# Kernel tuning notes

Measured on AMD Instinct MI355X. Metric: run time of the kernel, lower is better.

The kernel has to match this reference:

```python
import jax, jax.numpy as jnp
import numpy as np

B, S, H, V = 32, 512, 768, 30522
N_UPDATE, MAX_LEN = 3, 8
NEG_INF = -1e9


def setup_inputs() -> dict:
    key = jax.random.key(0)
    ks = jax.random.split(key, 12)
    x = jax.random.randint(ks[0], (B, S), 0, V, dtype=jnp.int32)
    decoder_input = jax.random.normal(ks[1], (B, N_UPDATE, H), dtype=jnp.float32)
    encoder_output = jax.random.normal(ks[2], (B, S, H), dtype=jnp.float32)
    hidden = jax.random.normal(ks[3], (1, B, H), dtype=jnp.float32)
    teacher = jax.random.randint(ks[4], (B, N_UPDATE, MAX_LEN), 0, V, dtype=jnp.int32)
    # tied embedding table, padding_idx=0 row zeroed
    embed_w = (jax.random.normal(ks[5], (V, H), dtype=jnp.float32) * 0.02).at[0].set(0.0)
    # GRU weights ~ N(0, initializer_range=0.02), biases zero (torch default biases exist; keep small random)
    gru_w_ih = jax.random.normal(ks[6], (3 * H, H), dtype=jnp.float32) * 0.02
    gru_w_hh = jax.random.normal(ks[7], (3 * H, H), dtype=jnp.float32) * 0.02
    gru_b_ih = jax.random.normal(ks[8], (3 * H,), dtype=jnp.float32) * 0.02
    gru_b_hh = jax.random.normal(ks[9], (3 * H,), dtype=jnp.float32) * 0.02
    wgen_w = jax.random.normal(ks[10], (1, 3 * H), dtype=jnp.float32) * 0.02
    wgen_b = jnp.zeros((1,), dtype=jnp.float32)
    return {"x": x, "decoder_input": decoder_input, "encoder_output": encoder_output,
            "hidden": hidden, "teacher": teacher, "embed_w": embed_w,
            "gru_w_ih": gru_w_ih, "gru_w_hh": gru_w_hh, "gru_b_ih": gru_b_ih,
            "gru_b_hh": gru_b_hh, "wgen_w": wgen_w, "wgen_b": wgen_b, "max_len": MAX_LEN}


def _gru_cell(w, h, w_ih, w_hh, b_ih, b_hh):
    # PyTorch GRU cell. w, h: [B, H]
    gi = w @ w_ih.T + b_ih  # [B, 3H]
    gh = h @ w_hh.T + b_hh
    i_r, i_z, i_n = jnp.split(gi, 3, axis=-1)
    h_r, h_z, h_n = jnp.split(gh, 3, axis=-1)
    r = jax.nn.sigmoid(i_r + h_r)
    z = jax.nn.sigmoid(i_z + h_z)
    n = jnp.tanh(i_n + r * h_n)
    return (1.0 - z) * n + z * h


def reference(x, decoder_input, encoder_output, hidden, teacher, embed_w,
              gru_w_ih, gru_w_hh, gru_b_ih, gru_b_hh, wgen_w, wgen_b, max_len):
    b, n_update, hid = decoder_input.shape
    vocab = embed_w.shape[0]
    mask = (x == 0)  # [B, S]
    bidx = jnp.arange(b)[:, None]

    # Teacher-forced inputs: step 0 of slot j uses decoder_input[:, j];
    # step k>0 uses embed(teacher[:, j, k-1]).
    teacher_emb = embed_w[teacher]                     # [B, nU, L, H]
    inputs = jnp.concatenate([decoder_input[:, :, None, :], teacher_emb[:, :, :-1, :]], axis=2)
    inputs = inputs.transpose(1, 2, 0, 3).reshape(n_update * max_len, b, hid)  # [nU*L, B, H]

    h0 = hidden[0]  # [B, H]

    def step(h, w):
        h = _gru_cell(w, h, gru_w_ih, gru_w_hh, gru_b_ih, gru_b_hh)
        attn_e = jnp.einsum('bsh,bh->bs', encoder_output, h)
        attn_e = jnp.where(mask, NEG_INF, attn_e)
        attn_history = jax.nn.softmax(attn_e, axis=-1)          # [B, S]
        attn_vocab = jax.nn.softmax(h @ embed_w.T, axis=-1)     # [B, V]
        context = jnp.einsum('bs,bsh->bh', attn_history, encoder_output)
        p_gen = jax.nn.sigmoid(jnp.concatenate([w, h, context], axis=-1) @ wgen_w.T + wgen_b)  # [B,1]
        p_ctx = jnp.zeros((b, vocab), dtype=attn_vocab.dtype).at[bidx, x].add(attn_history)
        p_final = p_gen * attn_vocab + (1.0 - p_gen) * p_ctx    # [B, V]
        return h, p_final

    _, p_all = jax.lax.scan(step, h0, inputs)                    # [nU*L, B, V]
    p_all = p_all.reshape(n_update, max_len, b, vocab).transpose(2, 0, 1, 3)
    return p_all  # [B, n_update, max_len, V]
```

## Files before the change

kernel.cpp:

```cpp
#include <hip/hip_runtime.h>
#include <cstdint>

#define B_  32
#define S_  512
#define H_  768
#define V_  30522
#define NT_ 24
#define H3  2304
#define NC4   (V_*H_/4)
#define NWALL (NT_*B_*H_)
#define NINIT (B_*H_)

#define GRU_NBLK 192
#define GRU_TPB  512
#define GRU_JPB  4
#define GRU_RPB  12

typedef unsigned short ushort_t;
typedef __attribute__((ext_vector_type(8))) short bf16x8;
typedef __attribute__((ext_vector_type(4))) float f32x4;

__device__ __forceinline__ ushort_t f2bf(float f){
  union { float f; unsigned u; } v; v.f = f;
  unsigned r = v.u + 0x7fffu + ((v.u >> 16) & 1u);
  return (ushort_t)(r >> 16);
}

__device__ __forceinline__ void load_lds_16B(const void* g, void* l){
  auto gp = reinterpret_cast<const __attribute__((address_space(1))) unsigned int*>(
      reinterpret_cast<uintptr_t>(g));
  auto lp = reinterpret_cast<__attribute__((address_space(3))) unsigned int*>(
      reinterpret_cast<uintptr_t>(l));
  __builtin_amdgcn_global_load_lds(gp, lp, 16, 0, 0);
}

__global__ void k_prep(const float* __restrict__ embed, const float* __restrict__ dec,
                       const int* __restrict__ teacher, const float* __restrict__ hidden,
                       ushort_t* __restrict__ E2, float* __restrict__ wall,
                       float* __restrict__ Hq, float* __restrict__ Hb,
                       float* __restrict__ pgacc, unsigned* __restrict__ flags){
  int idx = blockIdx.x * 256 + threadIdx.x;
  if (idx < NC4){
    float4 v = ((const float4*)embed)[idx];
    uint2 o;
    o.x = (unsigned)f2bf(v.x) | ((unsigned)f2bf(v.y) << 16);
    o.y = (unsigned)f2bf(v.z) | ((unsigned)f2bf(v.w) << 16);
    ((uint2*)E2)[idx] = o;
    return;
  }
  idx -= NC4;
  if (idx < NWALL){
    int k  = idx % H_;
    int rb = idx / H_;
    int t = rb >> 5, b = rb & 31;
    int jj = t >> 3, kk = t & 7;
    float v;
    if (kk == 0) v = dec[(b*3 + jj)*H_ + k];
    else { int tok = teacher[(b*3 + jj)*8 + kk - 1]; v = embed[(size_t)tok*H_ + k]; }
    wall[idx] = v;
    return;
  }
  idx -= NWALL;
  if (idx < NINIT){
    int b = idx / H_, k = idx % H_;
    float v = hidden[idx];
    Hb[idx] = v;
    Hq[((k >> 1)*B_ + b)*2 + (k & 1)] = v;
    return;
  }
  idx -= NINIT;
  if (idx < 768){ pgacc[idx] = 0.f; return; }
  idx -= 768;
  if (idx < 768) flags[idx] = 0u;
}

__global__ __launch_bounds__(256) void k_gi_gemm(const float* __restrict__ A, const float* __restrict__ Bm,
                                                 const float* __restrict__ bias, float* __restrict__ C){
  __shared__ float As[16][68];
  __shared__ float Bs[16][68];
  const int tid = threadIdx.x;
  const int tx = tid & 15, ty = tid >> 4;
  const int m0 = blockIdx.x * 64, n0 = blockIdx.y * 64;
  const int r = tid >> 2, kq = tid & 3;
  float acc[4][4] = {};
  for (int k0 = 0; k0 < 768; k0 += 16){
    float4 av = *(const float4*)&A [(size_t)(m0 + r)*768 + k0 + kq*4];
    float4 bv = *(const float4*)&Bm[(size_t)(n0 + r)*768 + k0 + kq*4];
    __syncthreads();
    As[kq*4+0][r] = av.x; As[kq*4+1][r] = av.y; As[kq*4+2][r] = av.z; As[kq*4+3][r] = av.w;
    Bs[kq*4+0][r] = bv.x; Bs[kq*4+1][r] = bv.y; Bs[kq*4+2][r] = bv.z; Bs[kq*4+3][r] = bv.w;
    __syncthreads();
#pragma unroll
    for (int kk = 0; kk < 16; ++kk){
      float4 a4 = *(const float4*)&As[kk][ty*4];
      float4 b4 = *(const float4*)&Bs[kk][tx*4];
      float aa[4] = {a4.x, a4.y, a4.z, a4.w};
      float bb[4] = {b4.x, b4.y, b4.z, b4.w};
#pragma unroll
      for (int i = 0; i < 4; ++i)
#pragma unroll
        for (int j = 0; j < 4; ++j)
          acc[i][j] = fmaf(aa[i], bb[j], acc[i][j]);
    }
  }
#pragma unroll
  for (int i = 0; i < 4; ++i){
    int m = m0 + ty*4 + i;
    int t = m >> 5, b = m & 31;
#pragma unroll
    for (int j = 0; j < 4; ++j){
      int n = n0 + tx*4 + j;
      C[((size_t)t*H3 + n)*32 + b] = acc[i][j] + bias[n];
    }
  }
}

__global__ __launch_bounds__(GRU_TPB) void k_gru_all(const float* __restrict__ gi, const float* __restrict__ whh,
                                                     const float* __restrict__ bhh, const float* __restrict__ hidden,
                                                     float* __restrict__ Hq, float* __restrict__ Hb,
                                                     ushort_t* __restrict__ A2, unsigned* __restrict__ flags){
  __shared__ float ws[GRU_RPB*768];
  __shared__ float red[16*392];
  __shared__ float bs[GRU_RPB];
  const int tid = threadIdx.x;
  const int j0 = blockIdx.x * GRU_JPB;

  for (int idx4 = tid; idx4 < GRU_RPB*192; idx4 += GRU_TPB){
    int r = idx4 / 192, k4 = idx4 % 192;
    int gate = r >> 2, jl = r & 3;
    *(float4*)&ws[r*768 + k4*4] = *(const float4*)&whh[(size_t)(gate*768 + j0 + jl)*768 + k4*4];
  }
  if (tid < GRU_RPB) bs[tid] = bhh[(tid >> 2)*768 + j0 + (tid & 3)];
  __syncthreads();

  const int ks = tid >> 5, b = tid & 31;
  const int jl = tid >> 5, bb = tid & 31;
  const int j  = j0 + (jl & 3);
  float hp = 0.f;
  if (tid < 128) hp = hidden[bb*768 + j];

  for (int t = 0; t < NT_; ++t){
    const unsigned long long* hsrc = (const unsigned long long*)(Hq + (size_t)t*24576);

    float ir = 0.f, iz = 0.f, inn = 0.f;
    if (tid < 128){
      const float* gi_t = gi + (size_t)t*H3*32;
      ir  = gi_t[(size_t)(       j)*32 + bb];
      iz  = gi_t[(size_t)(768  + j)*32 + bb];
      inn = gi_t[(size_t)(1536 + j)*32 + bb];
    }

    float acc[GRU_RPB];
#pragma unroll
    for (int r = 0; r < GRU_RPB; ++r) acc[r] = 0.f;
#pragma unroll
    for (int i = 0; i < 24; ++i){
      union { unsigned long long u; float f[2]; } cv;
      cv.u = __hip_atomic_load(&hsrc[(size_t)(ks*24 + i)*32 + b],
                               __ATOMIC_RELAXED, __HIP_MEMORY_SCOPE_AGENT);
      const float h0 = cv.f[0], h1 = cv.f[1];
#pragma unroll
      for (int r = 0; r < GRU_RPB; ++r){
        const float2 w2 = *(const float2*)&ws[r*768 + ks*48 + i*2];
        acc[r] += h0*w2.x + h1*w2.y;
      }
    }
#pragma unroll
    for (int r = 0; r < GRU_RPB; ++r) red[ks*392 + r*32 + b] = acc[r];
    __syncthreads();

    if (tid < 128){
      float aR = 0.f, aZ = 0.f, aN = 0.f;
#pragma unroll
      for (int k8 = 0; k8 < 16; ++k8){
        aR += red[k8*392 + (0*GRU_JPB + jl)*32 + bb];
        aZ += red[k8*392 + (1*GRU_JPB + jl)*32 + bb];
        aN += red[k8*392 + (2*GRU_JPB + jl)*32 + bb];
      }
      aR += bs[jl]; aZ += bs[GRU_JPB + jl]; aN += bs[2*GRU_JPB + jl];
      float rg = 1.f / (1.f + __expf(-(ir + aR)));
      float zg = 1.f / (1.f + __expf(-(iz + aZ)));
      float e2 = __expf(-2.f*(inn + rg * aN));
      float ng = (1.f - e2) / (1.f + e2);
      float hn = (1.f - zg)*ng + zg*hp;
      hp = hn;
      Hb[(size_t)(t+1)*24576 + bb*768 + j] = hn;
      A2[(size_t)(t*32 + bb)*768 + j] = f2bf(hn);
      if (t < NT_ - 1){
        union { float f; unsigned u; } hv; hv.f = hn;
        unsigned* hq32 = (unsigned*)(Hq + (size_t)(t+1)*24576);
        __hip_atomic_store(&hq32[((j >> 1)*32 + bb)*2 + (j & 1)], hv.u,
                           __ATOMIC_RELAXED, __HIP_MEMORY_SCOPE_AGENT);
      }
    }
    __syncthreads();

    if (t < NT_ - 1){
      if (tid == 0)
        __hip_atomic_store(&flags[(size_t)blockIdx.x*4], (unsigned)(t + 1),
                           __ATOMIC_RELAXED, __HIP_MEMORY_SCOPE_AGENT);
      if (tid < GRU_NBLK){
        unsigned spins = 0u;
        while (__hip_atomic_load(&flags[(size_t)tid*4], __ATOMIC_RELAXED,
                                 __HIP_MEMORY_SCOPE_AGENT) < (unsigned)(t + 1) &&
               ++spins < 20000000u)
          __builtin_amdgcn_s_sleep(1);
      }
      __syncthreads();
    }
  }
}

__global__ __launch_bounds__(256) void k_attn(const float* __restrict__ enc, const float* __restrict__ Hb1,
                                              float* __restrict__ ae){
  __shared__ float Es[64*36];
  __shared__ float Ht[24*36];
  const int b = blockIdx.x, s0 = blockIdx.y * 64;
  const int tid = threadIdx.x;
  const int s_l = tid & 63, tq = tid >> 6;
  const int r = tid >> 2, kq = tid & 3;
  float acc[6] = {0.f,0.f,0.f,0.f,0.f,0.f};
  for (int k0 = 0; k0 < 768; k0 += 32){
    __syncthreads();
    float4 e0 = *(const float4*)&enc[(size_t)(b*512 + s0 + r)*768 + k0 + kq*8];
    float4 e1 = *(const float4*)&enc[(size_t)(b*512 + s0 + r)*768 + k0 + kq*8 + 4];
    *(float4*)&Es[r*36 + kq*8]     = e0;
    *(float4*)&Es[r*36 + kq*8 + 4] = e1;
    if (tid < 192){
      int t = tid >> 3, k4 = tid & 7;
      *(float4*)&Ht[t*36 + k4*4] = *(const float4*)&Hb1[(size_t)t*24576 + b*768 + k0 + k4*4];
    }
    __syncthreads();
#pragma unroll
    for (int k4 = 0; k4 < 8; ++k4){
      float4 e = *(const float4*)&Es[s_l*36 + k4*4];
#pragma unroll
      for (int i = 0; i < 6; ++i){
        float4 h4 = *(const float4*)&Ht[(tq*6 + i)*36 + k4*4];
        acc[i] += e.x*h4.x + e.y*h4.y + e.z*h4.z + e.w*h4.w;
      }
    }
  }
#pragma unroll
  for (int i = 0; i < 6; ++i)
    ae[(size_t)((tq*6 + i)*32 + b)*512 + s0 + s_l] = acc[i];
}

__global__ __launch_bounds__(256) void k_attnsoft(const int* __restrict__ x, float* __restrict__ ae){
  const int row = blockIdx.x;
  const int b = row & 31;
  const int tid = threadIdx.x;
  __shared__ float red[256];
  float v0 = ae[(size_t)row*512 + tid];
  float v1 = ae[(size_t)row*512 + 256 + tid];
  if (x[b*512 + tid]        == 0) v0 = -1e9f;
  if (x[b*512 + 256 + tid]  == 0) v1 = -1e9f;
  float m = fmaxf(v0, v1);
  red[tid] = m; __syncthreads();
  for (int off = 128; off; off >>= 1){ if (tid < off) red[tid] = fmaxf(red[tid], red[tid+off]); __syncthreads(); }
  float M = red[0]; __syncthreads();
  float e0 = __expf(v0 - M), e1 = __expf(v1 - M);
  red[tid] = e0 + e1; __syncthreads();
  for (int off = 128; off; off >>= 1){ if (tid < off) red[tid] += red[tid+off]; __syncthreads(); }
  float inv = 1.f / red[0];
  ae[(size_t)row*512 + tid]       = e0 * inv;
  ae[(size_t)row*512 + 256 + tid] = e1 * inv;
}

__global__ __launch_bounds__(256) void k_ctx_pgen(const float* __restrict__ enc, const float* __restrict__ ah,
                                                  const float* __restrict__ wall, const float* __restrict__ Hb1,
                                                  const float* __restrict__ wg, float* __restrict__ pgacc){
  const int b = blockIdx.x;
  const int klane = threadIdx.x & 63;
  const int k = blockIdx.y * 64 + klane;
  const int tq = threadIdx.x >> 6;
  float acc[6] = {0.f,0.f,0.f,0.f,0.f,0.f};
  for (int s4 = 0; s4 < 512; s4 += 4){
    float e0 = enc[(size_t)(b*512 + s4 + 0)*768 + k];
    float e1 = enc[(size_t)(b*512 + s4 + 1)*768 + k];
    float e2 = enc[(size_t)(b*512 + s4 + 2)*768 + k];
    float e3 = enc[(size_t)(b*512 + s4 + 3)*768 + k];
#pragma unroll
    for (int i = 0; i < 6; ++i){
      float4 a4 = *(const float4*)&ah[(size_t)((tq*6 + i)*32 + b)*512 + s4];
      acc[i] = fmaf(a4.x, e0, acc[i]); acc[i] = fmaf(a4.y, e1, acc[i]);
      acc[i] = fmaf(a4.z, e2, acc[i]); acc[i] = fmaf(a4.w, e3, acc[i]);
    }
  }
  const float wgk = wg[k], wgh = wg[768 + k], wgc = wg[1536 + k];
#pragma unroll
  for (int i = 0; i < 6; ++i){
    const int t = tq*6 + i, row = t*32 + b;
    float p = acc[i]*wgc + wall[(size_t)row*768 + k]*wgk + Hb1[(size_t)t*24576 + b*768 + k]*wgh;
#pragma unroll
    for (int off = 32; off; off >>= 1) p += __shfl_down(p, off, 64);
    if (klane == 0) atomicAdd(&pgacc[row], p);
  }
}

__global__ __launch_bounds__(256) void k_vgemm(const ushort_t* __restrict__ A2, const ushort_t* __restrict__ E2,
                                               float* __restrict__ out){
  __shared__ ushort_t ldsA[128*64];
  __shared__ ushort_t ldsB[128*64];
  const int wg = blockIdx.x;
  const int xcd = wg & 7, qq = wg >> 3;
  const int ntile = (qq / 6) * 8 + xcd;
  const int mtile = qq % 6;
  const int tid = threadIdx.x;
  const int w = tid >> 6, lane = tid & 63;
  const int lrow = lane >> 3, lpos = lane & 7;
  const int wm = w >> 1, wn = w & 1;
  const int q = lane >> 4, fr = lane & 15;
  f32x4 acc[4][4];
  f32x4 zero = {0.f, 0.f, 0.f, 0.f};
#pragma unroll
  for (int a = 0; a < 4; ++a)
#pragma unroll
    for (int c = 0; c < 4; ++c) acc[a][c] = zero;

  for (int k0 = 0; k0 < 768; k0 += 64){
    __syncthreads();
#pragma unroll
    for (int i = 0; i < 4; ++i){
      int row = w*32 + i*8 + lrow;
      int c   = lpos ^ (row & 7);
      const ushort_t* srcA = A2 + (size_t)(mtile*128 + row)*768 + k0 + c*8;
      int brow = ntile*128 + row; if (brow > V_ - 1) brow = V_ - 1;
      const ushort_t* srcB = E2 + (size_t)brow*768 + k0 + c*8;
      load_lds_16B(srcA, &ldsA[row*64 + lpos*8]);
      load_lds_16B(srcB, &ldsB[row*64 + lpos*8]);
    }
    __builtin_amdgcn_s_waitcnt(0);
    __syncthreads();
#pragma unroll
    for (int s = 0; s < 2; ++s){
      bf16x8 af[4], bfr[4];
#pragma unroll
      for (int mt = 0; mt < 4; ++mt){
        int row = wm*64 + mt*16 + fr;
        int ch = (s*4 + q) ^ (row & 7);
        af[mt] = *(const bf16x8*)&ldsA[row*64 + ch*8];
      }
#pragma unroll
      for (int nt = 0; nt < 4; ++nt){
        int row = wn*64 + nt*16 + fr;
        int ch = (s*4 + q) ^ (row & 7);
        bfr[nt] = *(const bf16x8*)&ldsB[row*64 + ch*8];
      }
#pragma unroll
      for (int mt = 0; mt < 4; ++mt)
#pragma unroll
        for (int nt = 0; nt < 4; ++nt)
          acc[mt][nt] = __builtin_amdgcn_mfma_f32_16x16x32_bf16(af[mt], bfr[nt], acc[mt][nt], 0, 0, 0);
    }
  }
#pragma unroll
  for (int mt = 0; mt < 4; ++mt){
#pragma unroll
    for (int nt = 0; nt < 4; ++nt){
      int gn = ntile*128 + wn*64 + nt*16 + fr;
      if (gn >= V_) continue;
#pragma unroll
      for (int rg = 0; rg < 4; ++rg){
        int gm = mtile*128 + wm*64 + mt*16 + q*4 + rg;
        int t = gm >> 5, b = gm & 31;
        out[(size_t)(b*24 + t)*V_ + gn] = acc[mt][nt][rg];
      }
    }
  }
}

__global__ __launch_bounds__(512) void k_vsoft(float* __restrict__ out, const float* __restrict__ pgacc,
                                               const float* __restrict__ wgb){
  const int row = blockIdx.x;
  const int b = row / 24, t = row % 24;
  const float pg = 1.f / (1.f + __expf(-(pgacc[t*32 + b] + wgb[0])));
  const int tid = threadIdx.x;
  float* rp = out + (size_t)row * V_;
  const float4* rp4 = (const float4*)rp;
  float m = -3.0e38f, s = 0.f;
  for (int i = tid; i < 7630; i += 512){
    float4 v = rp4[i];
    float vm = fmaxf(fmaxf(v.x, v.y), fmaxf(v.z, v.w));
    float vs = __expf(v.x - vm) + __expf(v.y - vm) + __expf(v.z - vm) + __expf(v.w - vm);
    float nm = fmaxf(m, vm);
    s = s * __expf(m - nm) + vs * __expf(vm - nm);
    m = nm;
  }
  if (tid < 2){
    float v = rp[30520 + tid];
    float nm = fmaxf(m, v);
    s = s * __expf(m - nm) + __expf(v - nm);
    m = nm;
  }
#pragma unroll
  for (int off = 1; off < 64; off <<= 1){
    float m2 = __shfl_xor(m, off, 64), s2 = __shfl_xor(s, off, 64);
    float nm = fmaxf(m, m2);
    s = s*__expf(m - nm) + s2*__expf(m2 - nm);
    m = nm;
  }
  __shared__ float rm[8], rs[8];
  const int wid = tid >> 6;
  if ((tid & 63) == 0){ rm[wid] = m; rs[wid] = s; }
  __syncthreads();
  if (tid == 0){
    float M = rm[0], S = rs[0];
#pragma unroll
    for (int i = 1; i < 8; ++i){
      float m2 = rm[i], s2 = rs[i];
      float nm = fmaxf(M, m2);
      S = S*__expf(M - nm) + s2*__expf(m2 - nm);
      M = nm;
    }
    rm[0] = M; rs[0] = pg / S;
  }
  __syncthreads();
  const float M = rm[0], inv = rs[0];
  for (int i = tid; i < 7630; i += 512){
    float4 v = rp4[i];
    v.x = __expf(v.x - M) * inv;
    v.y = __expf(v.y - M) * inv;
    v.z = __expf(v.z - M) * inv;
    v.w = __expf(v.w - M) * inv;
    ((float4*)rp)[i] = v;
  }
  if (tid < 2) rp[30520 + tid] = __expf(rp[30520 + tid] - M) * inv;
}

__global__ void k_scatter(const float* __restrict__ ah, const float* __restrict__ pgacc,
                          const float* __restrict__ wgb, const int* __restrict__ x,
                          float* __restrict__ out){
  int idx = blockIdx.x * 256 + threadIdx.x;
  int s = idx & 511;
  int row = idx >> 9;
  int t = row >> 5, b = row & 31;
  float pg = 1.f / (1.f + __expf(-(pgacc[row] + wgb[0])));
  float val = ah[idx] * (1.f - pg);
  int col = x[b*512 + s];
  atomicAdd(&out[(size_t)(b*24 + t)*V_ + col], val);
}

extern "C" void kernel_launch(void* const* d_in, const int* in_sizes, int n_in,
                              void* d_out, int out_size, void* d_ws, size_t ws_size,
                              hipStream_t stream){
  (void)in_sizes; (void)n_in; (void)out_size; (void)ws_size;
  const int*   x      = (const int*)  d_in[0];
  const float* dec    = (const float*)d_in[1];
  const float* enc    = (const float*)d_in[2];
  const float* hidden = (const float*)d_in[3];
  const int*   teach  = (const int*)  d_in[4];
  const float* embed  = (const float*)d_in[5];
  const float* wih    = (const float*)d_in[6];
  const float* whh    = (const float*)d_in[7];
  const float* bih    = (const float*)d_in[8];
  const float* bhh    = (const float*)d_in[9];
  const float* wg     = (const float*)d_in[10];
  const float* wgb    = (const float*)d_in[11];
  float* out = (float*)d_out;

  char* p = (char*)d_ws;
  auto alloc = [&](size_t bytes){ void* r = (void*)p; p += (bytes + 255) & ~(size_t)255; return r; };
  ushort_t* E2  = (ushort_t*)alloc((size_t)V_ * H_ * 2);
  ushort_t* A2  = (ushort_t*)alloc((size_t)768 * 768 * 2);
  float* wall   = (float*)alloc((size_t)NT_ * B_ * H_ * 4);
  float* Hb     = (float*)alloc((size_t)(NT_+1) * B_ * H_ * 4);
  float* Hq     = (float*)alloc((size_t)(NT_+1) * B_ * H_ * 4);
  float* gi     = (float*)alloc((size_t)NT_ * B_ * H3 * 4);
  float* ae     = (float*)alloc((size_t)NT_ * B_ * S_ * 4);
  float* pgacc  = (float*)alloc(768 * 4);
  unsigned* flags = (unsigned*)alloc(768 * 4);

  const int prep_items  = NC4 + NWALL + NINIT + 768 + 768;
  const int prep_blocks = (prep_items + 255) / 256;

  k_prep<<<prep_blocks, 256, 0, stream>>>(embed, dec, teach, hidden, E2, wall, Hq, Hb, pgacc, flags);
  k_gi_gemm<<<dim3(12, 36), 256, 0, stream>>>(wall, wih, bih, gi);
  k_gru_all<<<GRU_NBLK, GRU_TPB, 0, stream>>>(gi, whh, bhh, hidden, Hq, Hb, A2, flags);
  k_attn<<<dim3(32, 8), 256, 0, stream>>>(enc, Hb + 24576, ae);
  k_attnsoft<<<768, 256, 0, stream>>>(x, ae);
  k_ctx_pgen<<<dim3(32, 12), 256, 0, stream>>>(enc, ae, wall, Hb + 24576, wg, pgacc);
  k_vgemm<<<1440, 256, 0, stream>>>(A2, E2, out);
  k_vsoft<<<768, 512, 0, stream>>>(out, pgacc, wgb);
  k_scatter<<<(NT_*B_*S_)/256, 256, 0, stream>>>(ae, pgacc, wgb, x, out);
}
```

Baseline: 731.2 us.

## Fuse input-gate GEMM into persistent GRU kernel using transposed inputs

Removes the separate k_gi_gemm launch and its gi buffer. The persistent GRU kernel now also stages W_ih rows in LDS and computes the input-gate projection each timestep from a transposed copy of the inputs written by k_prep. This saves one kernel launch and the gi round trip through memory. In exchange it doubles the per-step FMA and LDS traffic inside the latency-critical sequential loop and raises LDS use per block, which may hurt occupancy.

```diff
diff --git a/kernel.cpp b/kernel.cpp
--- a/kernel.cpp
+++ b/kernel.cpp
@@ -37,7 +37,7 @@
 __global__ void k_prep(const float* __restrict__ embed, const float* __restrict__ dec,
                        const int* __restrict__ teacher, const float* __restrict__ hidden,
                        ushort_t* __restrict__ E2, float* __restrict__ wall,
-                       float* __restrict__ Hq, float* __restrict__ Hb,
+                       float* __restrict__ wallT, float* __restrict__ Hq, float* __restrict__ Hb,
                        float* __restrict__ pgacc, unsigned* __restrict__ flags){
   int idx = blockIdx.x * 256 + threadIdx.x;
   if (idx < NC4){
@@ -58,6 +58,7 @@
     if (kk == 0) v = dec[(b*3 + jj)*H_ + k];
     else { int tok = teacher[(b*3 + jj)*8 + kk - 1]; v = embed[(size_t)tok*H_ + k]; }
     wall[idx] = v;
+    wallT[(size_t)t*24576 + ((k >> 1)*B_ + b)*2 + (k & 1)] = v;
     return;
   }
   idx -= NWALL;
@@ -74,63 +75,28 @@
   if (idx < 768) flags[idx] = 0u;
 }
 
-__global__ __launch_bounds__(256) void k_gi_gemm(const float* __restrict__ A, const float* __restrict__ Bm,
-                                                 const float* __restrict__ bias, float* __restrict__ C){
-  __shared__ float As[16][68];
-  __shared__ float Bs[16][68];
-  const int tid = threadIdx.x;
-  const int tx = tid & 15, ty = tid >> 4;
-  const int m0 = blockIdx.x * 64, n0 = blockIdx.y * 64;
-  const int r = tid >> 2, kq = tid & 3;
-  float acc[4][4] = {};
-  for (int k0 = 0; k0 < 768; k0 += 16){
-    float4 av = *(const float4*)&A [(size_t)(m0 + r)*768 + k0 + kq*4];
-    float4 bv = *(const float4*)&Bm[(size_t)(n0 + r)*768 + k0 + kq*4];
-    __syncthreads();
-    As[kq*4+0][r] = av.x; As[kq*4+1][r] = av.y; As[kq*4+2][r] = av.z; As[kq*4+3][r] = av.w;
-    Bs[kq*4+0][r] = bv.x; Bs[kq*4+1][r] = bv.y; Bs[kq*4+2][r] = bv.z; Bs[kq*4+3][r] = bv.w;
-    __syncthreads();
-#pragma unroll
-    for (int kk = 0; kk < 16; ++kk){
-      float4 a4 = *(const float4*)&As[kk][ty*4];
-      float4 b4 = *(const float4*)&Bs[kk][tx*4];
-      float aa[4] = {a4.x, a4.y, a4.z, a4.w};
-      float bb[4] = {b4.x, b4.y, b4.z, b4.w};
-#pragma unroll
-      for (int i = 0; i < 4; ++i)
-#pragma unroll
-        for (int j = 0; j < 4; ++j)
-          acc[i][j] = fmaf(aa[i], bb[j], acc[i][j]);
-    }
-  }
-#pragma unroll
-  for (int i = 0; i < 4; ++i){
-    int m = m0 + ty*4 + i;
-    int t = m >> 5, b = m & 31;
-#pragma unroll
-    for (int j = 0; j < 4; ++j){
-      int n = n0 + tx*4 + j;
-      C[((size_t)t*H3 + n)*32 + b] = acc[i][j] + bias[n];
-    }
-  }
-}
-
-__global__ __launch_bounds__(GRU_TPB) void k_gru_all(const float* __restrict__ gi, const float* __restrict__ whh,
+__global__ __launch_bounds__(GRU_TPB) void k_gru_all(const float* __restrict__ wallT, const float* __restrict__ wih,
+                                                     const float* __restrict__ whh, const float* __restrict__ bih,
                                                      const float* __restrict__ bhh, const float* __restrict__ hidden,
                                                      float* __restrict__ Hq, float* __restrict__ Hb,
                                                      ushort_t* __restrict__ A2, unsigned* __restrict__ flags){
-  __shared__ float ws[GRU_RPB*768];
-  __shared__ float red[16*392];
-  __shared__ float bs[GRU_RPB];
+  __shared__ float wsh[GRU_RPB*768];
+  __shared__ float wsi[GRU_RPB*768];
+  __shared__ float red[16*776];
+  __shared__ float bsh[GRU_RPB], bsi[GRU_RPB];
   const int tid = threadIdx.x;
   const int j0 = blockIdx.x * GRU_JPB;
 
   for (int idx4 = tid; idx4 < GRU_RPB*192; idx4 += GRU_TPB){
     int r = idx4 / 192, k4 = idx4 % 192;
     int gate = r >> 2, jl = r & 3;
-    *(float4*)&ws[r*768 + k4*4] = *(const float4*)&whh[(size_t)(gate*768 + j0 + jl)*768 + k4*4];
-  }
-  if (tid < GRU_RPB) bs[tid] = bhh[(tid >> 2)*768 + j0 + (tid & 3)];
+    *(float4*)&wsh[r*768 + k4*4] = *(const float4*)&whh[(size_t)(gate*768 + j0 + jl)*768 + k4*4];
+    *(float4*)&wsi[r*768 + k4*4] = *(const float4*)&wih[(size_t)(gate*768 + j0 + jl)*768 + k4*4];
+  }
+  if (tid < GRU_RPB){
+    bsh[tid] = bhh[(tid >> 2)*768 + j0 + (tid & 3)];
+    bsi[tid] = bih[(tid >> 2)*768 + j0 + (tid & 3)];
+  }
   __syncthreads();
 
   const int ks = tid >> 5, b = tid & 31;
@@ -141,43 +107,43 @@
 
   for (int t = 0; t < NT_; ++t){
     const unsigned long long* hsrc = (const unsigned long long*)(Hq + (size_t)t*24576);
-
-    float ir = 0.f, iz = 0.f, inn = 0.f;
-    if (tid < 128){
-      const float* gi_t = gi + (size_t)t*H3*32;
-      ir  = gi_t[(size_t)(       j)*32 + bb];
-      iz  = gi_t[(size_t)(768  + j)*32 + bb];
-      inn = gi_t[(size_t)(1536 + j)*32 + bb];
-    }
-
-    float acc[GRU_RPB];
-#pragma unroll
-    for (int r = 0; r < GRU_RPB; ++r) acc[r] = 0.f;
-#pragma unroll
+    const float2* wsrc = (const float2*)(wallT + (size_t)t*24576);
+
+    float acch[GRU_RPB], acci[GRU_RPB];
+#pragma unroll
+    for (int r = 0; r < GRU_RPB; ++r){ acch[r] = 0.f; acci[r] = 0.f; }
+#pragma unroll 4
     for (int i = 0; i < 24; ++i){
       union { unsigned long long u; float f[2]; } cv;
       cv.u = __hip_atomic_load(&hsrc[(size_t)(ks*24 + i)*32 + b],
                                __ATOMIC_RELAXED, __HIP_MEMORY_SCOPE_AGENT);
+      const float2 wv = wsrc[(size_t)(ks*24 + i)*32 + b];
       const float h0 = cv.f[0], h1 = cv.f[1];
 #pragma unroll
       for (int r = 0; r < GRU_RPB; ++r){
-        const float2 w2 = *(const float2*)&ws[r*768 + ks*48 + i*2];
-        acc[r] += h0*w2.x + h1*w2.y;
-      }
-    }
-#pragma unroll
-    for (int r = 0; r < GRU_RPB; ++r) red[ks*392 + r*32 + b] = acc[r];
+        const float2 wh = *(const float2*)&wsh[r*768 + ks*48 + i*2];
+        const float2 wi = *(const float2*)&wsi[r*768 + ks*48 + i*2];
+        acch[r] += h0*wh.x + h1*wh.y;
+        acci[r] += wv.x*wi.x + wv.y*wi.y;
+      }
+    }
+#pragma unroll
+    for (int r = 0; r < GRU_RPB; ++r){
+      red[ks*776 + r*32 + b]             = acch[r];
+      red[ks*776 + (GRU_RPB + r)*32 + b] = acci[r];
+    }
     __syncthreads();
 
     if (tid < 128){
-      float aR = 0.f, aZ = 0.f, aN = 0.f;
+      float aR = 0.f, aZ = 0.f, aN = 0.f, iR = 0.f, iZ = 0.f, iN = 0.f;
 #pragma unroll
       for (int k8 = 0; k8 < 16; ++k8){
-        aR += red[k8*392 + (0*GRU_JPB + jl)*32 + bb];
-        aZ += red[k8*392 + (1*GRU_JPB + jl)*32 + bb];
-        aN += red[k8*392 + (2*GRU_JPB + jl)*32 + bb];
-      }
-      aR += bs[jl]; aZ += bs[GRU_JPB + jl]; aN += bs[2*GRU_JPB + jl];
+        const float* rb_ = &red[k8*776 + jl*32 + bb];
+        aR += rb_[0*128]; aZ += rb_[1*128]; aN += rb_[2*128];
+        iR += rb_[3*128]; iZ += rb_[4*128]; iN += rb_[5*128];
+      }
+      aR += bsh[jl]; aZ += bsh[4 + jl]; aN += bsh[8 + jl];
+      const float ir = iR + bsi[jl], iz = iZ + bsi[4 + jl], inn = iN + bsi[8 + jl];
       float rg = 1.f / (1.f + __expf(-(ir + aR)));
       float zg = 1.f / (1.f + __expf(-(iz + aZ)));
       float e2 = __expf(-2.f*(inn + rg * aN));
@@ -464,9 +430,9 @@
   ushort_t* E2  = (ushort_t*)alloc((size_t)V_ * H_ * 2);
   ushort_t* A2  = (ushort_t*)alloc((size_t)768 * 768 * 2);
   float* wall   = (float*)alloc((size_t)NT_ * B_ * H_ * 4);
+  float* wallT  = (float*)alloc((size_t)NT_ * B_ * H_ * 4);
   float* Hb     = (float*)alloc((size_t)(NT_+1) * B_ * H_ * 4);
   float* Hq     = (float*)alloc((size_t)(NT_+1) * B_ * H_ * 4);
-  float* gi     = (float*)alloc((size_t)NT_ * B_ * H3 * 4);
   float* ae     = (float*)alloc((size_t)NT_ * B_ * S_ * 4);
   float* pgacc  = (float*)alloc(768 * 4);
   unsigned* flags = (unsigned*)alloc(768 * 4);
@@ -474,9 +440,8 @@
   const int prep_items  = NC4 + NWALL + NINIT + 768 + 768;
   const int prep_blocks = (prep_items + 255) / 256;
 
-  k_prep<<<prep_blocks, 256, 0, stream>>>(embed, dec, teach, hidden, E2, wall, Hq, Hb, pgacc, flags);
-  k_gi_gemm<<<dim3(12, 36), 256, 0, stream>>>(wall, wih, bih, gi);
-  k_gru_all<<<GRU_NBLK, GRU_TPB, 0, stream>>>(gi, whh, bhh, hidden, Hq, Hb, A2, flags);
+  k_prep<<<prep_blocks, 256, 0, stream>>>(embed, dec, teach, hidden, E2, wall, wallT, Hq, Hb, pgacc, flags);
+  k_gru_all<<<GRU_NBLK, GRU_TPB, 0, stream>>>(wallT, wih, whh, bih, bhh, hidden, Hq, Hb, A2, flags);
   k_attn<<<dim3(32, 8), 256, 0, stream>>>(enc, Hb + 24576, ae);
   k_attnsoft<<<768, 256, 0, stream>>>(x, ae);
   k_ctx_pgen<<<dim3(32, 12), 256, 0, stream>>>(enc, ae, wall, Hb + 24576, wg, pgacc);
```

Result: faster. 706.4 us (-3.4%).
